# Performance work log

Hardware: AMD Instinct MI355X
Metric: run time of the kernel (lower is better)

## Reference

```python
import jax, jax.numpy as jnp
import numpy as np

E = 1024      # embed_dim
H = 16        # num_heads
HD = E // H   # head_dim = 64


def setup_inputs() -> dict:
    key = jax.random.key(0)
    ks = jax.random.split(key, 8)
    T, B, S = 1024, 4, 1024
    return {
        "query": jax.random.normal(ks[0], (T, B, E), jnp.float32),
        "key": jax.random.normal(ks[1], (S, B, E), jnp.float32),
        "value": jax.random.normal(ks[2], (S, B, E), jnp.float32),
        "attn_mask": jax.random.normal(ks[3], (T, S), jnp.float32),
        "key_padding_mask": jax.random.randint(ks[4], (B, S), 0, 2, jnp.int32),
        "in_proj_weight": jax.random.normal(ks[5], (3 * E, E), jnp.float32) * 0.02,
        "in_proj_bias": jnp.zeros((3 * E,), jnp.float32),
        "out_w": jax.random.normal(ks[6], (E, E), jnp.float32) * 0.02,
        "out_b": jnp.zeros((E,), jnp.float32),
    }


def reference(query, key, value, attn_mask, key_padding_mask,
              in_proj_weight, in_proj_bias, out_w, out_b):
    T, B, _ = query.shape
    S = key.shape[0]
    w_q, w_k, w_v = jnp.split(in_proj_weight, 3, axis=0)   # each [E, E]
    b_q, b_k, b_v = jnp.split(in_proj_bias, 3, axis=0)
    q = query @ w_q.T + b_q                                # [T, B, E]
    k = key @ w_k.T + b_k                                  # [S, B, E]
    v = value @ w_v.T + b_v                                # [S, B, E]
    # [len, B, E] -> [B*H, len, HD]
    q = q.reshape(T, B * H, HD).transpose(1, 0, 2) / jnp.sqrt(jnp.float32(HD))
    k = k.reshape(S, B * H, HD).transpose(1, 0, 2)
    v = v.reshape(S, B * H, HD).transpose(1, 0, 2)
    scores = jnp.einsum('bth,bsh->bts', q, k)              # [B*H, T, S]
    scores = scores + attn_mask[None]                      # float additive mask
    pad = key_padding_mask.astype(bool)                    # [B, S]
    pad = jnp.broadcast_to(pad[:, None, None, :], (B, H, 1, S)).reshape(B * H, 1, S)
    scores = jnp.where(pad, -jnp.inf, scores)
    weights = jax.nn.softmax(scores, axis=-1)              # dropout p=0 -> identity
    out = jnp.einsum('bts,bsh->bth', weights, v)           # [B*H, T, HD]
    out = out.transpose(1, 0, 2).reshape(T, B, E)
    out = out @ out_w.T + out_b
    weights_avg = weights.reshape(B, H, T, S).mean(axis=1) # sum/H == mean
    return out, weights_avg
```

## Files before the change

kernel.cpp:

```cpp
#include <hip/hip_runtime.h>
#include <stdint.h>

typedef short bf16x8 __attribute__((ext_vector_type(8)));
typedef float f32x4  __attribute__((ext_vector_type(4)));

#define LOG2E_F 1.4426950408889634f
#define QSCALE_F 0.1803368801111204f

__device__ __forceinline__ unsigned short f2bf(float f) {
    unsigned int u = __float_as_uint(f);
    return (unsigned short)((u + 0x7FFFu + ((u >> 16) & 1u)) >> 16);
}

__device__ __forceinline__ unsigned short f2bfu(float f) {
    return (unsigned short)((__float_as_uint(f) + 0x8000u) >> 16);
}

__device__ __forceinline__ uint4 pack8(float4 a, float4 b) {
    union { unsigned short us[8]; uint4 v; } p;
    p.us[0] = f2bf(a.x); p.us[1] = f2bf(a.y); p.us[2] = f2bf(a.z); p.us[3] = f2bf(a.w);
    p.us[4] = f2bf(b.x); p.us[5] = f2bf(b.y); p.us[6] = f2bf(b.z); p.us[7] = f2bf(b.w);
    return p.v;
}

__global__ __launch_bounds__(256)
void cvt_kernel(const float* __restrict__ q, const float* __restrict__ k,
                const float* __restrict__ v, const float* __restrict__ w,
                const float* __restrict__ ow,
                uint4* __restrict__ Xb, uint4* __restrict__ Wb, uint4* __restrict__ OWb)
{
    const unsigned g = blockIdx.x * 256 + threadIdx.x;
    const float* src;
    uint4* dst;
    if (g < 1572864u) {
        dst = Xb + g;
        if (g < 524288u)        src = q + (size_t)g * 8;
        else if (g < 1048576u)  src = k + (size_t)(g - 524288u) * 8;
        else                    src = v + (size_t)(g - 1048576u) * 8;
    } else if (g < 1966080u) {
        src = w + (size_t)(g - 1572864u) * 8;
        dst = Wb + (g - 1572864u);
    } else {
        src = ow + (size_t)(g - 1966080u) * 8;
        dst = OWb + (g - 1966080u);
    }
    float4 a = *(const float4*)src;
    float4 b = *(const float4*)(src + 4);
    *dst = pack8(a, b);
}

__global__ __launch_bounds__(256)
void qkv_proj_kernel(const unsigned short* __restrict__ Xb, const unsigned short* __restrict__ Wb,
                     const float* __restrict__ bias,
                     unsigned short* __restrict__ Qb, unsigned short* __restrict__ Kb,
                     unsigned short* __restrict__ Vtb)
{
    const int z = blockIdx.z;
    const int j   = blockIdx.x;
    const int xcd = j & 7, idx = j >> 3;
    const int row0 = ((xcd << 2) + (idx >> 3)) * 128;
    const int col0 = (idx & 7) * 128;
    const int wofs = z << 10;

    const unsigned short* A = Xb + (size_t)z * 4194304;
    const unsigned short* B = Wb;

    __shared__ __align__(16) unsigned short As[128 * 72];
    __shared__ __align__(16) unsigned short Bs[128 * 72];

    const int tid  = threadIdx.x;
    const int lane = tid & 63;
    const int wv   = tid >> 6;
    const int wr   = wv >> 1, wc = wv & 1;

    const f32x4 zero4 = {0.f, 0.f, 0.f, 0.f};
    f32x4 acc[4][4];
#pragma unroll
    for (int m = 0; m < 4; ++m)
#pragma unroll
        for (int n = 0; n < 4; ++n) acc[m][n] = zero4;

    const int srow = tid >> 1;
    const int scol = (tid & 1) << 5;
    const int arow = wr * 64 + (lane & 15);
    const int brow = wc * 64 + (lane & 15);
    const int kof  = (lane >> 4) << 3;

    const unsigned short* pa = A + (size_t)(row0 + srow) * 1024 + scol;
    const unsigned short* pb = B + (size_t)(wofs + col0 + srow) * 1024 + scol;
    uint4 ra0 = *(const uint4*)(pa + 0),  ra1 = *(const uint4*)(pa + 8);
    uint4 ra2 = *(const uint4*)(pa + 16), ra3 = *(const uint4*)(pa + 24);
    uint4 rb0 = *(const uint4*)(pb + 0),  rb1 = *(const uint4*)(pb + 8);
    uint4 rb2 = *(const uint4*)(pb + 16), rb3 = *(const uint4*)(pb + 24);

    for (int k0 = 0; k0 < 1024; k0 += 64) {
        __syncthreads();
        *(uint4*)&As[srow * 72 + scol]      = ra0;
        *(uint4*)&As[srow * 72 + scol + 8]  = ra1;
        *(uint4*)&As[srow * 72 + scol + 16] = ra2;
        *(uint4*)&As[srow * 72 + scol + 24] = ra3;
        *(uint4*)&Bs[srow * 72 + scol]      = rb0;
        *(uint4*)&Bs[srow * 72 + scol + 8]  = rb1;
        *(uint4*)&Bs[srow * 72 + scol + 16] = rb2;
        *(uint4*)&Bs[srow * 72 + scol + 24] = rb3;
        __syncthreads();

        if (k0 < 960) {
            pa = A + (size_t)(row0 + srow) * 1024 + k0 + 64 + scol;
            pb = B + (size_t)(wofs + col0 + srow) * 1024 + k0 + 64 + scol;
            ra0 = *(const uint4*)(pa + 0);  ra1 = *(const uint4*)(pa + 8);
            ra2 = *(const uint4*)(pa + 16); ra3 = *(const uint4*)(pa + 24);
            rb0 = *(const uint4*)(pb + 0);  rb1 = *(const uint4*)(pb + 8);
            rb2 = *(const uint4*)(pb + 16); rb3 = *(const uint4*)(pb + 24);
        }

#pragma unroll
        for (int kk = 0; kk < 2; ++kk) {
            bf16x8 af[4], bfr[4];
#pragma unroll
            for (int m = 0; m < 4; ++m)
                af[m] = *(const bf16x8*)&As[(arow + m * 16) * 72 + kk * 32 + kof];
#pragma unroll
            for (int n = 0; n < 4; ++n)
                bfr[n] = *(const bf16x8*)&Bs[(brow + n * 16) * 72 + kk * 32 + kof];
#pragma unroll
            for (int m = 0; m < 4; ++m)
#pragma unroll
                for (int n = 0; n < 4; ++n)
                    acc[m][n] = __builtin_amdgcn_mfma_f32_16x16x32_bf16(af[m], bfr[n], acc[m][n], 0, 0, 0);
        }
    }

    const int ccol = lane & 15;
    const int crow = (lane >> 4) << 2;
#pragma unroll
    for (int n = 0; n < 4; ++n) {
        const int gc   = col0 + wc * 64 + n * 16 + ccol;
        const float bv = bias[wofs + gc];
        const int head = gc >> 6, d = gc & 63;
#pragma unroll
        for (int m = 0; m < 4; ++m) {
#pragma unroll
            for (int r = 0; r < 4; ++r) {
                const int gr = row0 + wr * 64 + m * 16 + crow + r;
                const int t  = gr >> 2, b = gr & 3;
                const int bh = (b << 4) + head;
                float vv = acc[m][n][r] + bv;
                if (z == 0)      Qb [((size_t)bh << 16) + ((size_t)t << 6) + d]  = f2bf(vv * QSCALE_F);
                else if (z == 1) Kb [((size_t)bh << 16) + ((size_t)t << 6) + d]  = f2bf(vv);
                else             Vtb[((size_t)bh << 16) + ((size_t)d << 10) + t] = f2bf(vv);
            }
        }
    }
}

__global__ __launch_bounds__(256)
void flash_kernel(const unsigned short* __restrict__ Qb, const unsigned short* __restrict__ Kb,
                  const unsigned short* __restrict__ Vtb, const float* __restrict__ attn_mask,
                  const int* __restrict__ padmask,
                  float* __restrict__ rl_buf, unsigned short* __restrict__ attn_out)
{
    const int j   = blockIdx.x;
    const int xcd = j & 7, idx = j >> 3;
    const int bh  = xcd * 8 + (idx >> 4);
    const int t0  = (idx & 15) << 6;
    const int b   = bh >> 4, h = bh & 15;

    __shared__ __align__(16) unsigned short Ks[64 * 72];
    __shared__ __align__(16) unsigned short Vs[64 * 72];
    __shared__ __align__(16) unsigned short Ps[64 * 72];

    const int tid  = threadIdx.x;
    const int lane = tid & 63;
    const int wv   = tid >> 6;
    const int kof  = (lane >> 4) << 3;
    const int c16  = lane & 15;

    const unsigned short* Qbase = Qb  + ((size_t)bh << 16);
    const unsigned short* Kbase = Kb  + ((size_t)bh << 16);
    const unsigned short* Vbase = Vtb + ((size_t)bh << 16);

    bf16x8 qf[2];
#pragma unroll
    for (int kk = 0; kk < 2; ++kk)
        qf[kk] = *(const bf16x8*)(Qbase + ((size_t)(t0 + wv * 16 + c16) << 6) + kk * 32 + kof);

    const bf16x8 ones = {16256, 16256, 16256, 16256, 16256, 16256, 16256, 16256};

    const f32x4 zero4 = {0.f, 0.f, 0.f, 0.f};
    f32x4 acco[4];
#pragma unroll
    for (int nd = 0; nd < 4; ++nd) acco[nd] = zero4;
    f32x4 acc_l = zero4;

    const int srow_st = tid >> 2;
    const int scol_st = (tid & 3) << 4;

    const unsigned short* kp = Kbase + ((size_t)srow_st << 6) + scol_st;
    const unsigned short* vp = Vbase + ((size_t)srow_st << 10) + scol_st;
    uint4 kr0 = *(const uint4*)kp, kr1 = *(const uint4*)(kp + 8);
    uint4 vr0 = *(const uint4*)vp, vr1 = *(const uint4*)(vp + 8);

    for (int s0 = 0; s0 < 1024; s0 += 64) {
        __syncthreads();
        *(uint4*)&Ks[srow_st * 72 + scol_st]     = kr0;
        *(uint4*)&Ks[srow_st * 72 + scol_st + 8] = kr1;
        *(uint4*)&Vs[srow_st * 72 + scol_st]     = vr0;
        *(uint4*)&Vs[srow_st * 72 + scol_st + 8] = vr1;
        __syncthreads();

        if (s0 < 960) {
            kp = Kbase + ((size_t)(s0 + 64 + srow_st) << 6) + scol_st;
            vp = Vbase + ((size_t)srow_st << 10) + (s0 + 64) + scol_st;
            kr0 = *(const uint4*)kp; kr1 = *(const uint4*)(kp + 8);
            vr0 = *(const uint4*)vp; vr1 = *(const uint4*)(vp + 8);
        }

        f32x4 accs[4];
#pragma unroll
        for (int n = 0; n < 4; ++n) accs[n] = zero4;
#pragma unroll
        for (int n = 0; n < 4; ++n) {
            bf16x8 kf0 = *(const bf16x8*)&Ks[(n * 16 + c16) * 72 + kof];
            bf16x8 kf1 = *(const bf16x8*)&Ks[(n * 16 + c16) * 72 + 32 + kof];
            accs[n] = __builtin_amdgcn_mfma_f32_16x16x32_bf16(qf[0], kf0, accs[n], 0, 0, 0);
            accs[n] = __builtin_amdgcn_mfma_f32_16x16x32_bf16(qf[1], kf1, accs[n], 0, 0, 0);
        }

        int pad_s[4];
#pragma unroll
        for (int n = 0; n < 4; ++n)
            pad_s[n] = padmask[(b << 10) + s0 + n * 16 + c16];

        const int rbase = wv * 16 + ((lane >> 4) << 2);
#pragma unroll
        for (int r = 0; r < 4; ++r) {
            const float* mp = attn_mask + (size_t)(t0 + rbase + r) * 1024 + s0 + c16;
            float x0 = fmaf(mp[ 0], LOG2E_F, accs[0][r]);
            float x1 = fmaf(mp[16], LOG2E_F, accs[1][r]);
            float x2 = fmaf(mp[32], LOG2E_F, accs[2][r]);
            float x3 = fmaf(mp[48], LOG2E_F, accs[3][r]);
            if (pad_s[0]) x0 = -1e30f;
            if (pad_s[1]) x1 = -1e30f;
            if (pad_s[2]) x2 = -1e30f;
            if (pad_s[3]) x3 = -1e30f;
            const float p0 = __builtin_amdgcn_exp2f(x0);
            const float p1 = __builtin_amdgcn_exp2f(x1);
            const float p2 = __builtin_amdgcn_exp2f(x2);
            const float p3 = __builtin_amdgcn_exp2f(x3);
            const int prow = rbase + r;
            Ps[prow * 72 +  0 + c16] = f2bfu(p0);
            Ps[prow * 72 + 16 + c16] = f2bfu(p1);
            Ps[prow * 72 + 32 + c16] = f2bfu(p2);
            Ps[prow * 72 + 48 + c16] = f2bfu(p3);
        }

#pragma unroll
        for (int kk2 = 0; kk2 < 2; ++kk2) {
            bf16x8 pf = *(const bf16x8*)&Ps[(wv * 16 + c16) * 72 + kk2 * 32 + kof];
#pragma unroll
            for (int nd = 0; nd < 4; ++nd) {
                bf16x8 vf = *(const bf16x8*)&Vs[(nd * 16 + c16) * 72 + kk2 * 32 + kof];
                acco[nd] = __builtin_amdgcn_mfma_f32_16x16x32_bf16(pf, vf, acco[nd], 0, 0, 0);
            }
            acc_l = __builtin_amdgcn_mfma_f32_16x16x32_bf16(pf, ones, acc_l, 0, 0, 0);
        }
    }

#pragma unroll
    for (int r = 0; r < 4; ++r) {
        const int t = t0 + wv * 16 + ((lane >> 4) << 2) + r;
        const float rl = 1.0f / acc_l[r];
        if (c16 == 0)
            rl_buf[(bh << 10) + t] = rl;
#pragma unroll
        for (int nd = 0; nd < 4; ++nd) {
            const int d = nd * 16 + c16;
            attn_out[((size_t)t * 4 + b) * 1024 + h * 64 + d] = f2bf(acco[nd][r] * rl);
        }
    }
}

__global__ __launch_bounds__(256)
void wavg_kernel(const unsigned short* __restrict__ Qb, const unsigned short* __restrict__ Kb,
                 const float* __restrict__ attn_mask, const int* __restrict__ padmask,
                 const float* __restrict__ rl_buf, float* __restrict__ wout)
{
    const int j   = blockIdx.x;
    const int xcd = j & 7;
    const int b   = xcd >> 1;
    const int rr  = ((j >> 3) << 1) + (xcd & 1);
    const int t0  = (rr >> 4) << 6;
    const int s0  = (rr & 15) << 6;

    __shared__ __align__(16) unsigned short Qs[64 * 72];
    __shared__ __align__(16) unsigned short Ks2[64 * 72];

    const int tid  = threadIdx.x;
    const int lane = tid & 63;
    const int wv   = tid >> 6;
    const int wr   = wv >> 1, wc = wv & 1;
    const int kof  = (lane >> 4) << 3;
    const int srow_st = tid >> 2;
    const int scol_st = (tid & 3) << 4;

    const int t_base = t0 + wr * 32 + ((lane >> 4) << 2);
    const int s_base = s0 + wc * 32 + (lane & 15);

    int pad2[2];
#pragma unroll
    for (int nn = 0; nn < 2; ++nn) pad2[nn] = padmask[(b << 10) + s_base + nn * 16];

    float maskv[2][2][4];
#pragma unroll
    for (int mm = 0; mm < 2; ++mm)
#pragma unroll
        for (int r = 0; r < 4; ++r)
#pragma unroll
            for (int nn = 0; nn < 2; ++nn)
                maskv[mm][nn][r] = attn_mask[(size_t)(t_base + mm * 16 + r) * 1024 + s_base + nn * 16] * LOG2E_F;

    float wsum[2][2][4];
#pragma unroll
    for (int mm = 0; mm < 2; ++mm)
#pragma unroll
        for (int nn = 0; nn < 2; ++nn)
#pragma unroll
            for (int r = 0; r < 4; ++r) wsum[mm][nn][r] = 0.f;

    for (int h = 0; h < 16; ++h) {
        const int bh = (b << 4) + h;
        __syncthreads();
        {
            const unsigned short* qp = Qb + ((size_t)bh << 16) + ((size_t)(t0 + srow_st) << 6) + scol_st;
            *(uint4*)&Qs[srow_st * 72 + scol_st]     = *(const uint4*)qp;
            *(uint4*)&Qs[srow_st * 72 + scol_st + 8] = *(const uint4*)(qp + 8);
            const unsigned short* kp = Kb + ((size_t)bh << 16) + ((size_t)(s0 + srow_st) << 6) + scol_st;
            *(uint4*)&Ks2[srow_st * 72 + scol_st]     = *(const uint4*)kp;
            *(uint4*)&Ks2[srow_st * 72 + scol_st + 8] = *(const uint4*)(kp + 8);
        }
        __syncthreads();

        float rlv[2][4];
#pragma unroll
        for (int mm = 0; mm < 2; ++mm)
#pragma unroll
            for (int r = 0; r < 4; ++r)
                rlv[mm][r] = rl_buf[(bh << 10) + t_base + mm * 16 + r];

        const f32x4 zero4 = {0.f, 0.f, 0.f, 0.f};
        f32x4 accs[2][2];
#pragma unroll
        for (int mm = 0; mm < 2; ++mm)
#pragma unroll
            for (int nn = 0; nn < 2; ++nn) accs[mm][nn] = zero4;
#pragma unroll
        for (int nn = 0; nn < 2; ++nn) {
            bf16x8 kf0 = *(const bf16x8*)&Ks2[(wc * 32 + nn * 16 + (lane & 15)) * 72 + kof];
            bf16x8 kf1 = *(const bf16x8*)&Ks2[(wc * 32 + nn * 16 + (lane & 15)) * 72 + 32 + kof];
#pragma unroll
            for (int mm = 0; mm < 2; ++mm) {
                bf16x8 qf0 = *(const bf16x8*)&Qs[(wr * 32 + mm * 16 + (lane & 15)) * 72 + kof];
                bf16x8 qf1 = *(const bf16x8*)&Qs[(wr * 32 + mm * 16 + (lane & 15)) * 72 + 32 + kof];
                accs[mm][nn] = __builtin_amdgcn_mfma_f32_16x16x32_bf16(qf0, kf0, accs[mm][nn], 0, 0, 0);
                accs[mm][nn] = __builtin_amdgcn_mfma_f32_16x16x32_bf16(qf1, kf1, accs[mm][nn], 0, 0, 0);
            }
        }
#pragma unroll
        for (int mm = 0; mm < 2; ++mm)
#pragma unroll
            for (int nn = 0; nn < 2; ++nn)
#pragma unroll
                for (int r = 0; r < 4; ++r)
                    if (!pad2[nn]) {
                        float x = accs[mm][nn][r] + maskv[mm][nn][r];
                        wsum[mm][nn][r] += __builtin_amdgcn_exp2f(x) * rlv[mm][r];
                    }
    }

#pragma unroll
    for (int mm = 0; mm < 2; ++mm)
#pragma unroll
        for (int nn = 0; nn < 2; ++nn)
#pragma unroll
            for (int r = 0; r < 4; ++r)
                wout[((size_t)b << 20) + (size_t)(t_base + mm * 16 + r) * 1024 + s_base + nn * 16]
                    = wsum[mm][nn][r] * 0.0625f;
}

__global__ __launch_bounds__(256)
void out_proj_kernel(const unsigned short* __restrict__ A, const unsigned short* __restrict__ Wb,
                     const float* __restrict__ bias, float* __restrict__ out)
{
    const int j   = blockIdx.x;
    const int xcd = j & 7, idx = j >> 3;
    const int row0 = ((xcd << 2) + (idx >> 3)) * 128;
    const int col0 = (idx & 7) * 128;

    __shared__ __align__(16) unsigned short As[128 * 72];
    __shared__ __align__(16) unsigned short Bs[128 * 72];

    const int tid  = threadIdx.x;
    const int lane = tid & 63;
    const int wv   = tid >> 6;
    const int wr   = wv >> 1, wc = wv & 1;

    const f32x4 zero4 = {0.f, 0.f, 0.f, 0.f};
    f32x4 acc[4][4];
#pragma unroll
    for (int m = 0; m < 4; ++m)
#pragma unroll
        for (int n = 0; n < 4; ++n) acc[m][n] = zero4;

    const int srow = tid >> 1;
    const int scol = (tid & 1) << 5;
    const int arow = wr * 64 + (lane & 15);
    const int brow = wc * 64 + (lane & 15);
    const int kof  = (lane >> 4) << 3;

    const unsigned short* pa = A  + (size_t)(row0 + srow) * 1024 + scol;
    const unsigned short* pb = Wb + (size_t)(col0 + srow) * 1024 + scol;
    uint4 ra0 = *(const uint4*)(pa + 0),  ra1 = *(const uint4*)(pa + 8);
    uint4 ra2 = *(const uint4*)(pa + 16), ra3 = *(const uint4*)(pa + 24);
    uint4 rb0 = *(const uint4*)(pb + 0),  rb1 = *(const uint4*)(pb + 8);
    uint4 rb2 = *(const uint4*)(pb + 16), rb3 = *(const uint4*)(pb + 24);

    for (int k0 = 0; k0 < 1024; k0 += 64) {
        __syncthreads();
        *(uint4*)&As[srow * 72 + scol]      = ra0;
        *(uint4*)&As[srow * 72 + scol + 8]  = ra1;
        *(uint4*)&As[srow * 72 + scol + 16] = ra2;
        *(uint4*)&As[srow * 72 + scol + 24] = ra3;
        *(uint4*)&Bs[srow * 72 + scol]      = rb0;
        *(uint4*)&Bs[srow * 72 + scol + 8]  = rb1;
        *(uint4*)&Bs[srow * 72 + scol + 16] = rb2;
        *(uint4*)&Bs[srow * 72 + scol + 24] = rb3;
        __syncthreads();

        if (k0 < 960) {
            pa = A  + (size_t)(row0 + srow) * 1024 + k0 + 64 + scol;
            pb = Wb + (size_t)(col0 + srow) * 1024 + k0 + 64 + scol;
            ra0 = *(const uint4*)(pa + 0);  ra1 = *(const uint4*)(pa + 8);
            ra2 = *(const uint4*)(pa + 16); ra3 = *(const uint4*)(pa + 24);
            rb0 = *(const uint4*)(pb + 0);  rb1 = *(const uint4*)(pb + 8);
            rb2 = *(const uint4*)(pb + 16); rb3 = *(const uint4*)(pb + 24);
        }

#pragma unroll
        for (int kk = 0; kk < 2; ++kk) {
            bf16x8 af[4], bfr[4];
#pragma unroll
            for (int m = 0; m < 4; ++m)
                af[m] = *(const bf16x8*)&As[(arow + m * 16) * 72 + kk * 32 + kof];
#pragma unroll
            for (int n = 0; n < 4; ++n)
                bfr[n] = *(const bf16x8*)&Bs[(brow + n * 16) * 72 + kk * 32 + kof];
#pragma unroll
            for (int m = 0; m < 4; ++m)
#pragma unroll
                for (int n = 0; n < 4; ++n)
                    acc[m][n] = __builtin_amdgcn_mfma_f32_16x16x32_bf16(af[m], bfr[n], acc[m][n], 0, 0, 0);
        }
    }

    const int ccol = lane & 15;
    const int crow = (lane >> 4) << 2;
#pragma unroll
    for (int n = 0; n < 4; ++n) {
        const int gc   = col0 + wc * 64 + n * 16 + ccol;
        const float bv = bias[gc];
#pragma unroll
        for (int m = 0; m < 4; ++m) {
#pragma unroll
            for (int r = 0; r < 4; ++r) {
                const int gr = row0 + wr * 64 + m * 16 + crow + r;
                out[(size_t)gr * 1024 + gc] = acc[m][n][r] + bv;
            }
        }
    }
}

extern "C" void kernel_launch(void* const* d_in, const int* in_sizes, int n_in,
                              void* d_out, int out_size, void* d_ws, size_t ws_size,
                              hipStream_t stream)
{
    const float* query     = (const float*)d_in[0];
    const float* key       = (const float*)d_in[1];
    const float* value     = (const float*)d_in[2];
    const float* attn_mask = (const float*)d_in[3];
    const int*   padmask   = (const int*)  d_in[4];
    const float* in_proj_w = (const float*)d_in[5];
    const float* in_proj_b = (const float*)d_in[6];
    const float* out_w     = (const float*)d_in[7];
    const float* out_b     = (const float*)d_in[8];

    float* out  = (float*)d_out;
    float* wavg = out + 4194304;

    char* ws = (char*)d_ws;
    unsigned short* Qb     = (unsigned short*)(ws);
    unsigned short* Kb     = (unsigned short*)(ws + 8388608);
    unsigned short* Vtb    = (unsigned short*)(ws + 16777216);
    unsigned short* Xb     = (unsigned short*)(ws + 25165824);
    unsigned short* attn_o = (unsigned short*)(ws + 25165824);
    unsigned short* Wb     = (unsigned short*)(ws + 50331648);
    unsigned short* OWb    = (unsigned short*)(ws + 56623104);
    float*          rl_buf = (float*)(ws + 58720256);

    cvt_kernel<<<dim3(8192), 256, 0, stream>>>(query, key, value, in_proj_w, out_w,
                                               (uint4*)Xb, (uint4*)Wb, (uint4*)OWb);
    qkv_proj_kernel<<<dim3(256, 1, 3), 256, 0, stream>>>(Xb, Wb, in_proj_b, Qb, Kb, Vtb);
    flash_kernel<<<dim3(1024), 256, 0, stream>>>(Qb, Kb, Vtb, attn_mask, padmask,
                                                 rl_buf, attn_o);
    wavg_kernel<<<dim3(1024), 256, 0, stream>>>(Qb, Kb, attn_mask, padmask,
                                                rl_buf, wavg);
    out_proj_kernel<<<dim3(256), 256, 0, stream>>>(attn_o, OWb, out_b, out);
}
```

Measured before the change: 158.6 us.

## Double-buffer K/V and Q/K tiles in flash and wavg kernels, enlarge flash blocks

The flash kernel now runs 512-thread blocks covering 128 query rows, with double-buffered K/V shared tiles. The attention mask and padding values for the next tile are prefetched into registers, and s_setprio is raised around the MFMA sections. The wavg kernel likewise double-buffers its Q/K tiles across heads, which drops one barrier per iteration. The aim is to hide global-load latency behind MFMA work and cut synchronisation, at the cost of more registers and LDS per block, which may lower occupancy.

Result: slower. 200.1 us (+26.2%).

```diff
diff --git a/kernel.cpp b/kernel.cpp
--- a/kernel.cpp
+++ b/kernel.cpp
@@ -154,7 +154,7 @@
     }
 }
 
-__global__ __launch_bounds__(256)
+__global__ __launch_bounds__(512, 4)
 void flash_kernel(const unsigned short* __restrict__ Qb, const unsigned short* __restrict__ Kb,
                   const unsigned short* __restrict__ Vtb, const float* __restrict__ attn_mask,
                   const int* __restrict__ padmask,
@@ -162,13 +162,13 @@
 {
     const int j   = blockIdx.x;
     const int xcd = j & 7, idx = j >> 3;
-    const int bh  = xcd * 8 + (idx >> 4);
-    const int t0  = (idx & 15) << 6;
+    const int bh  = xcd * 8 + (idx >> 3);
+    const int t0  = (idx & 7) << 7;
     const int b   = bh >> 4, h = bh & 15;
 
-    __shared__ __align__(16) unsigned short Ks[64 * 72];
-    __shared__ __align__(16) unsigned short Vs[64 * 72];
-    __shared__ __align__(16) unsigned short Ps[64 * 72];
+    __shared__ __align__(16) unsigned short Ks[2][64 * 72];
+    __shared__ __align__(16) unsigned short Vs[2][64 * 72];
+    __shared__ __align__(16) unsigned short Ps[128 * 72];
 
     const int tid  = threadIdx.x;
     const int lane = tid & 63;
@@ -193,57 +193,77 @@
     for (int nd = 0; nd < 4; ++nd) acco[nd] = zero4;
     f32x4 acc_l = zero4;
 
-    const int srow_st = tid >> 2;
-    const int scol_st = (tid & 3) << 4;
-
-    const unsigned short* kp = Kbase + ((size_t)srow_st << 6) + scol_st;
-    const unsigned short* vp = Vbase + ((size_t)srow_st << 10) + scol_st;
-    uint4 kr0 = *(const uint4*)kp, kr1 = *(const uint4*)(kp + 8);
-    uint4 vr0 = *(const uint4*)vp, vr1 = *(const uint4*)(vp + 8);
-
-    for (int s0 = 0; s0 < 1024; s0 += 64) {
-        __syncthreads();
-        *(uint4*)&Ks[srow_st * 72 + scol_st]     = kr0;
-        *(uint4*)&Ks[srow_st * 72 + scol_st + 8] = kr1;
-        *(uint4*)&Vs[srow_st * 72 + scol_st]     = vr0;
-        *(uint4*)&Vs[srow_st * 72 + scol_st + 8] = vr1;
-        __syncthreads();
-
-        if (s0 < 960) {
-            kp = Kbase + ((size_t)(s0 + 64 + srow_st) << 6) + scol_st;
-            vp = Vbase + ((size_t)srow_st << 10) + (s0 + 64) + scol_st;
-            kr0 = *(const uint4*)kp; kr1 = *(const uint4*)(kp + 8);
-            vr0 = *(const uint4*)vp; vr1 = *(const uint4*)(vp + 8);
+    const int srow = tid >> 3;
+    const int scol = (tid & 7) << 3;
+
+    const int tr = t0 + wv * 16 + ((lane >> 4) << 2);
+
+    uint4 kreg = *(const uint4*)(Kbase + ((size_t)srow << 6) + scol);
+    uint4 vreg = *(const uint4*)(Vbase + ((size_t)srow << 10) + scol);
+    float mreg[2][4][4];
+    int   preg[2][4];
+#pragma unroll
+    for (int n = 0; n < 4; ++n) preg[0][n] = padmask[(b << 10) + n * 16 + c16];
+#pragma unroll
+    for (int r = 0; r < 4; ++r)
+#pragma unroll
+        for (int n = 0; n < 4; ++n)
+            mreg[0][r][n] = attn_mask[(size_t)(tr + r) * 1024 + n * 16 + c16];
+
+    *(uint4*)&Ks[0][srow * 72 + scol] = kreg;
+    *(uint4*)&Vs[0][srow * 72 + scol] = vreg;
+    kreg = *(const uint4*)(Kbase + ((size_t)(64 + srow) << 6) + scol);
+    vreg = *(const uint4*)(Vbase + ((size_t)srow << 10) + 64 + scol);
+    __syncthreads();
+
+#pragma unroll 2
+    for (int it = 0; it < 16; ++it) {
+        const int cur = it & 1;
+
+        if (it < 15) {
+            *(uint4*)&Ks[cur ^ 1][srow * 72 + scol] = kreg;
+            *(uint4*)&Vs[cur ^ 1][srow * 72 + scol] = vreg;
+        }
+        if (it < 14) {
+            const int s2 = (it + 2) << 6;
+            kreg = *(const uint4*)(Kbase + ((size_t)(s2 + srow) << 6) + scol);
+            vreg = *(const uint4*)(Vbase + ((size_t)srow << 10) + s2 + scol);
+        }
+        if (it < 15) {
+            const int s1 = (it + 1) << 6;
+#pragma unroll
+            for (int n = 0; n < 4; ++n) preg[cur ^ 1][n] = padmask[(b << 10) + s1 + n * 16 + c16];
+#pragma unroll
+            for (int r = 0; r < 4; ++r)
+#pragma unroll
+                for (int n = 0; n < 4; ++n)
+                    mreg[cur ^ 1][r][n] = attn_mask[(size_t)(tr + r) * 1024 + s1 + n * 16 + c16];
         }
 
         f32x4 accs[4];
 #pragma unroll
         for (int n = 0; n < 4; ++n) accs[n] = zero4;
+        __builtin_amdgcn_s_setprio(1);
 #pragma unroll
         for (int n = 0; n < 4; ++n) {
-            bf16x8 kf0 = *(const bf16x8*)&Ks[(n * 16 + c16) * 72 + kof];
-            bf16x8 kf1 = *(const bf16x8*)&Ks[(n * 16 + c16) * 72 + 32 + kof];
+            bf16x8 kf0 = *(const bf16x8*)&Ks[cur][(n * 16 + c16) * 72 + kof];
+            bf16x8 kf1 = *(const bf16x8*)&Ks[cur][(n * 16 + c16) * 72 + 32 + kof];
             accs[n] = __builtin_amdgcn_mfma_f32_16x16x32_bf16(qf[0], kf0, accs[n], 0, 0, 0);
             accs[n] = __builtin_amdgcn_mfma_f32_16x16x32_bf16(qf[1], kf1, accs[n], 0, 0, 0);
         }
-
-        int pad_s[4];
-#pragma unroll
-        for (int n = 0; n < 4; ++n)
-            pad_s[n] = padmask[(b << 10) + s0 + n * 16 + c16];
+        __builtin_amdgcn_s_setprio(0);
 
         const int rbase = wv * 16 + ((lane >> 4) << 2);
 #pragma unroll
         for (int r = 0; r < 4; ++r) {
-            const float* mp = attn_mask + (size_t)(t0 + rbase + r) * 1024 + s0 + c16;
-            float x0 = fmaf(mp[ 0], LOG2E_F, accs[0][r]);
-            float x1 = fmaf(mp[16], LOG2E_F, accs[1][r]);
-            float x2 = fmaf(mp[32], LOG2E_F, accs[2][r]);
-            float x3 = fmaf(mp[48], LOG2E_F, accs[3][r]);
-            if (pad_s[0]) x0 = -1e30f;
-            if (pad_s[1]) x1 = -1e30f;
-            if (pad_s[2]) x2 = -1e30f;
-            if (pad_s[3]) x3 = -1e30f;
+            float x0 = fmaf(mreg[cur][r][0], LOG2E_F, accs[0][r]);
+            float x1 = fmaf(mreg[cur][r][1], LOG2E_F, accs[1][r]);
+            float x2 = fmaf(mreg[cur][r][2], LOG2E_F, accs[2][r]);
+            float x3 = fmaf(mreg[cur][r][3], LOG2E_F, accs[3][r]);
+            if (preg[cur][0]) x0 = -1e30f;
+            if (preg[cur][1]) x1 = -1e30f;
+            if (preg[cur][2]) x2 = -1e30f;
+            if (preg[cur][3]) x3 = -1e30f;
             const float p0 = __builtin_amdgcn_exp2f(x0);
             const float p1 = __builtin_amdgcn_exp2f(x1);
             const float p2 = __builtin_amdgcn_exp2f(x2);
@@ -255,16 +275,20 @@
             Ps[prow * 72 + 48 + c16] = f2bfu(p3);
         }
 
+        __builtin_amdgcn_s_setprio(1);
 #pragma unroll
         for (int kk2 = 0; kk2 < 2; ++kk2) {
             bf16x8 pf = *(const bf16x8*)&Ps[(wv * 16 + c16) * 72 + kk2 * 32 + kof];
 #pragma unroll
             for (int nd = 0; nd < 4; ++nd) {
-                bf16x8 vf = *(const bf16x8*)&Vs[(nd * 16 + c16) * 72 + kk2 * 32 + kof];
+                bf16x8 vf = *(const bf16x8*)&Vs[cur][(nd * 16 + c16) * 72 + kk2 * 32 + kof];
                 acco[nd] = __builtin_amdgcn_mfma_f32_16x16x32_bf16(pf, vf, acco[nd], 0, 0, 0);
             }
             acc_l = __builtin_amdgcn_mfma_f32_16x16x32_bf16(pf, ones, acc_l, 0, 0, 0);
         }
+        __builtin_amdgcn_s_setprio(0);
+
+        if (it < 15) __syncthreads();
     }
 
 #pragma unroll
@@ -293,8 +317,8 @@
     const int t0  = (rr >> 4) << 6;
     const int s0  = (rr & 15) << 6;
 
-    __shared__ __align__(16) unsigned short Qs[64 * 72];
-    __shared__ __align__(16) unsigned short Ks2[64 * 72];
+    __shared__ __align__(16) unsigned short Qs[2][64 * 72];
+    __shared__ __align__(16) unsigned short Ks2[2][64 * 72];
 
     const int tid  = threadIdx.x;
     const int lane = tid & 63;
@@ -328,18 +352,42 @@
 #pragma unroll
             for (int r = 0; r < 4; ++r) wsum[mm][nn][r] = 0.f;
 
+    const unsigned short* qsrc = Qb + ((size_t)(t0 + srow_st) << 6) + scol_st;
+    const unsigned short* ksrc = Kb + ((size_t)(s0 + srow_st) << 6) + scol_st;
+    const size_t bh0 = (size_t)(b << 4) << 16;
+
+    uint4 q0 = *(const uint4*)(qsrc + bh0);
+    uint4 q1 = *(const uint4*)(qsrc + bh0 + 8);
+    uint4 k0 = *(const uint4*)(ksrc + bh0);
+    uint4 k1 = *(const uint4*)(ksrc + bh0 + 8);
+    *(uint4*)&Qs[0][srow_st * 72 + scol_st]      = q0;
+    *(uint4*)&Qs[0][srow_st * 72 + scol_st + 8]  = q1;
+    *(uint4*)&Ks2[0][srow_st * 72 + scol_st]     = k0;
+    *(uint4*)&Ks2[0][srow_st * 72 + scol_st + 8] = k1;
+    q0 = *(const uint4*)(qsrc + bh0 + 65536);
+    q1 = *(const uint4*)(qsrc + bh0 + 65536 + 8);
+    k0 = *(const uint4*)(ksrc + bh0 + 65536);
+    k1 = *(const uint4*)(ksrc + bh0 + 65536 + 8);
+    __syncthreads();
+
+#pragma unroll 2
     for (int h = 0; h < 16; ++h) {
-        const int bh = (b << 4) + h;
-        __syncthreads();
-        {
-            const unsigned short* qp = Qb + ((size_t)bh << 16) + ((size_t)(t0 + srow_st) << 6) + scol_st;
-            *(uint4*)&Qs[srow_st * 72 + scol_st]     = *(const uint4*)qp;
-            *(uint4*)&Qs[srow_st * 72 + scol_st + 8] = *(const uint4*)(qp + 8);
-            const unsigned short* kp = Kb + ((size_t)bh << 16) + ((size_t)(s0 + srow_st) << 6) + scol_st;
-            *(uint4*)&Ks2[srow_st * 72 + scol_st]     = *(const uint4*)kp;
-            *(uint4*)&Ks2[srow_st * 72 + scol_st + 8] = *(const uint4*)(kp + 8);
-        }
-        __syncthreads();
+        const int cur = h & 1;
+        const int bh  = (b << 4) + h;
+
+        if (h < 15) {
+            *(uint4*)&Qs[cur ^ 1][srow_st * 72 + scol_st]      = q0;
+            *(uint4*)&Qs[cur ^ 1][srow_st * 72 + scol_st + 8]  = q1;
+            *(uint4*)&Ks2[cur ^ 1][srow_st * 72 + scol_st]     = k0;
+            *(uint4*)&Ks2[cur ^ 1][srow_st * 72 + scol_st + 8] = k1;
+        }
+        if (h < 14) {
+            const size_t of = bh0 + (size_t)(h + 2) * 65536;
+            q0 = *(const uint4*)(qsrc + of);
+            q1 = *(const uint4*)(qsrc + of + 8);
+            k0 = *(const uint4*)(ksrc + of);
+            k1 = *(const uint4*)(ksrc + of + 8);
+        }
 
         float rlv[2][4];
 #pragma unroll
@@ -356,12 +404,12 @@
             for (int nn = 0; nn < 2; ++nn) accs[mm][nn] = zero4;
 #pragma unroll
         for (int nn = 0; nn < 2; ++nn) {
-            bf16x8 kf0 = *(const bf16x8*)&Ks2[(wc * 32 + nn * 16 + (lane & 15)) * 72 + kof];
-            bf16x8 kf1 = *(const bf16x8*)&Ks2[(wc * 32 + nn * 16 + (lane & 15)) * 72 + 32 + kof];
+            bf16x8 kf0 = *(const bf16x8*)&Ks2[cur][(wc * 32 + nn * 16 + (lane & 15)) * 72 + kof];
+            bf16x8 kf1 = *(const bf16x8*)&Ks2[cur][(wc * 32 + nn * 16 + (lane & 15)) * 72 + 32 + kof];
 #pragma unroll
             for (int mm = 0; mm < 2; ++mm) {
-                bf16x8 qf0 = *(const bf16x8*)&Qs[(wr * 32 + mm * 16 + (lane & 15)) * 72 + kof];
-                bf16x8 qf1 = *(const bf16x8*)&Qs[(wr * 32 + mm * 16 + (lane & 15)) * 72 + 32 + kof];
+                bf16x8 qf0 = *(const bf16x8*)&Qs[cur][(wr * 32 + mm * 16 + (lane & 15)) * 72 + kof];
+                bf16x8 qf1 = *(const bf16x8*)&Qs[cur][(wr * 32 + mm * 16 + (lane & 15)) * 72 + 32 + kof];
                 accs[mm][nn] = __builtin_amdgcn_mfma_f32_16x16x32_bf16(qf0, kf0, accs[mm][nn], 0, 0, 0);
                 accs[mm][nn] = __builtin_amdgcn_mfma_f32_16x16x32_bf16(qf1, kf1, accs[mm][nn], 0, 0, 0);
             }
@@ -376,6 +424,8 @@
                         float x = accs[mm][nn][r] + maskv[mm][nn][r];
                         wsum[mm][nn][r] += __builtin_amdgcn_exp2f(x) * rlv[mm][r];
                     }
+
+        if (h < 15) __syncthreads();
     }
 
 #pragma unroll
@@ -510,8 +560,8 @@
     cvt_kernel<<<dim3(8192), 256, 0, stream>>>(query, key, value, in_proj_w, out_w,
                                                (uint4*)Xb, (uint4*)Wb, (uint4*)OWb);
     qkv_proj_kernel<<<dim3(256, 1, 3), 256, 0, stream>>>(Xb, Wb, in_proj_b, Qb, Kb, Vtb);
-    flash_kernel<<<dim3(1024), 256, 0, stream>>>(Qb, Kb, Vtb, attn_mask, padmask,
-                                                 rl_buf, attn_o);
+    flash_kernel<<<dim3(512), 512, 0, stream>>>(Qb, Kb, Vtb, attn_mask, padmask,
+                                                rl_buf, attn_o);
     wavg_kernel<<<dim3(1024), 256, 0, stream>>>(Qb, Kb, attn_mask, padmask,
                                                 rl_buf, wavg);
     out_proj_kernel<<<dim3(256), 256, 0, stream>>>(attn_o, OWb, out_b, out);
```

## Load K/V/Q MFMA fragments directly from global memory, drop LDS staging and barriers

Applied to the files above, without the earlier changes.

In both the flash attention kernel and the weight-averaging kernel, the shared-memory staging of K, V (and Q in wavg) is removed. MFMA operands are now read straight from global memory, relying on L1/L2 caching, and the two __syncthreads per iteration are gone. s_setprio raises wave priority around the MFMA sections. This removes the LDS round trip and barrier stalls, but drops the register prefetch double-buffering and makes each wave issue redundant global loads that may expose memory latency.

Result: slower. 271.7 us (+71.3%).

```diff
diff --git a/kernel.cpp b/kernel.cpp
--- a/kernel.cpp
+++ b/kernel.cpp
@@ -166,8 +166,6 @@
     const int t0  = (idx & 15) << 6;
     const int b   = bh >> 4, h = bh & 15;
 
-    __shared__ __align__(16) unsigned short Ks[64 * 72];
-    __shared__ __align__(16) unsigned short Vs[64 * 72];
     __shared__ __align__(16) unsigned short Ps[64 * 72];
 
     const int tid  = threadIdx.x;
@@ -193,49 +191,32 @@
     for (int nd = 0; nd < 4; ++nd) acco[nd] = zero4;
     f32x4 acc_l = zero4;
 
-    const int srow_st = tid >> 2;
-    const int scol_st = (tid & 3) << 4;
-
-    const unsigned short* kp = Kbase + ((size_t)srow_st << 6) + scol_st;
-    const unsigned short* vp = Vbase + ((size_t)srow_st << 10) + scol_st;
-    uint4 kr0 = *(const uint4*)kp, kr1 = *(const uint4*)(kp + 8);
-    uint4 vr0 = *(const uint4*)vp, vr1 = *(const uint4*)(vp + 8);
+    const int rbase = wv * 16 + ((lane >> 4) << 2);
+    const int tr    = t0 + rbase;
 
     for (int s0 = 0; s0 < 1024; s0 += 64) {
-        __syncthreads();
-        *(uint4*)&Ks[srow_st * 72 + scol_st]     = kr0;
-        *(uint4*)&Ks[srow_st * 72 + scol_st + 8] = kr1;
-        *(uint4*)&Vs[srow_st * 72 + scol_st]     = vr0;
-        *(uint4*)&Vs[srow_st * 72 + scol_st + 8] = vr1;
-        __syncthreads();
-
-        if (s0 < 960) {
-            kp = Kbase + ((size_t)(s0 + 64 + srow_st) << 6) + scol_st;
-            vp = Vbase + ((size_t)srow_st << 10) + (s0 + 64) + scol_st;
-            kr0 = *(const uint4*)kp; kr1 = *(const uint4*)(kp + 8);
-            vr0 = *(const uint4*)vp; vr1 = *(const uint4*)(vp + 8);
-        }
-
         f32x4 accs[4];
 #pragma unroll
         for (int n = 0; n < 4; ++n) accs[n] = zero4;
+        __builtin_amdgcn_s_setprio(1);
 #pragma unroll
         for (int n = 0; n < 4; ++n) {
-            bf16x8 kf0 = *(const bf16x8*)&Ks[(n * 16 + c16) * 72 + kof];
-            bf16x8 kf1 = *(const bf16x8*)&Ks[(n * 16 + c16) * 72 + 32 + kof];
+            const unsigned short* kr = Kbase + ((size_t)(s0 + n * 16 + c16) << 6) + kof;
+            bf16x8 kf0 = *(const bf16x8*)(kr);
+            bf16x8 kf1 = *(const bf16x8*)(kr + 32);
             accs[n] = __builtin_amdgcn_mfma_f32_16x16x32_bf16(qf[0], kf0, accs[n], 0, 0, 0);
             accs[n] = __builtin_amdgcn_mfma_f32_16x16x32_bf16(qf[1], kf1, accs[n], 0, 0, 0);
         }
+        __builtin_amdgcn_s_setprio(0);
 
         int pad_s[4];
 #pragma unroll
         for (int n = 0; n < 4; ++n)
             pad_s[n] = padmask[(b << 10) + s0 + n * 16 + c16];
 
-        const int rbase = wv * 16 + ((lane >> 4) << 2);
 #pragma unroll
         for (int r = 0; r < 4; ++r) {
-            const float* mp = attn_mask + (size_t)(t0 + rbase + r) * 1024 + s0 + c16;
+            const float* mp = attn_mask + (size_t)(tr + r) * 1024 + s0 + c16;
             float x0 = fmaf(mp[ 0], LOG2E_F, accs[0][r]);
             float x1 = fmaf(mp[16], LOG2E_F, accs[1][r]);
             float x2 = fmaf(mp[32], LOG2E_F, accs[2][r]);
@@ -255,21 +236,23 @@
             Ps[prow * 72 + 48 + c16] = f2bfu(p3);
         }
 
+        __builtin_amdgcn_s_setprio(1);
 #pragma unroll
         for (int kk2 = 0; kk2 < 2; ++kk2) {
             bf16x8 pf = *(const bf16x8*)&Ps[(wv * 16 + c16) * 72 + kk2 * 32 + kof];
 #pragma unroll
             for (int nd = 0; nd < 4; ++nd) {
-                bf16x8 vf = *(const bf16x8*)&Vs[(nd * 16 + c16) * 72 + kk2 * 32 + kof];
+                bf16x8 vf = *(const bf16x8*)(Vbase + ((size_t)(nd * 16 + c16) << 10) + s0 + kk2 * 32 + kof);
                 acco[nd] = __builtin_amdgcn_mfma_f32_16x16x32_bf16(pf, vf, acco[nd], 0, 0, 0);
             }
             acc_l = __builtin_amdgcn_mfma_f32_16x16x32_bf16(pf, ones, acc_l, 0, 0, 0);
         }
+        __builtin_amdgcn_s_setprio(0);
     }
 
 #pragma unroll
     for (int r = 0; r < 4; ++r) {
-        const int t = t0 + wv * 16 + ((lane >> 4) << 2) + r;
+        const int t = t0 + rbase + r;
         const float rl = 1.0f / acc_l[r];
         if (c16 == 0)
             rl_buf[(bh << 10) + t] = rl;
@@ -293,19 +276,15 @@
     const int t0  = (rr >> 4) << 6;
     const int s0  = (rr & 15) << 6;
 
-    __shared__ __align__(16) unsigned short Qs[64 * 72];
-    __shared__ __align__(16) unsigned short Ks2[64 * 72];
-
     const int tid  = threadIdx.x;
     const int lane = tid & 63;
     const int wv   = tid >> 6;
     const int wr   = wv >> 1, wc = wv & 1;
     const int kof  = (lane >> 4) << 3;
-    const int srow_st = tid >> 2;
-    const int scol_st = (tid & 3) << 4;
+    const int c16  = lane & 15;
 
     const int t_base = t0 + wr * 32 + ((lane >> 4) << 2);
-    const int s_base = s0 + wc * 32 + (lane & 15);
+    const int s_base = s0 + wc * 32 + c16;
 
     int pad2[2];
 #pragma unroll
@@ -328,18 +307,12 @@
 #pragma unroll
             for (int r = 0; r < 4; ++r) wsum[mm][nn][r] = 0.f;
 
+    const f32x4 zero4 = {0.f, 0.f, 0.f, 0.f};
+
     for (int h = 0; h < 16; ++h) {
         const int bh = (b << 4) + h;
-        __syncthreads();
-        {
-            const unsigned short* qp = Qb + ((size_t)bh << 16) + ((size_t)(t0 + srow_st) << 6) + scol_st;
-            *(uint4*)&Qs[srow_st * 72 + scol_st]     = *(const uint4*)qp;
-            *(uint4*)&Qs[srow_st * 72 + scol_st + 8] = *(const uint4*)(qp + 8);
-            const unsigned short* kp = Kb + ((size_t)bh << 16) + ((size_t)(s0 + srow_st) << 6) + scol_st;
-            *(uint4*)&Ks2[srow_st * 72 + scol_st]     = *(const uint4*)kp;
-            *(uint4*)&Ks2[srow_st * 72 + scol_st + 8] = *(const uint4*)(kp + 8);
-        }
-        __syncthreads();
+        const unsigned short* Qh = Qb + ((size_t)bh << 16);
+        const unsigned short* Kh = Kb + ((size_t)bh << 16);
 
         float rlv[2][4];
 #pragma unroll
@@ -348,24 +321,29 @@
             for (int r = 0; r < 4; ++r)
                 rlv[mm][r] = rl_buf[(bh << 10) + t_base + mm * 16 + r];
 
-        const f32x4 zero4 = {0.f, 0.f, 0.f, 0.f};
         f32x4 accs[2][2];
 #pragma unroll
         for (int mm = 0; mm < 2; ++mm)
 #pragma unroll
             for (int nn = 0; nn < 2; ++nn) accs[mm][nn] = zero4;
+
+        __builtin_amdgcn_s_setprio(1);
 #pragma unroll
         for (int nn = 0; nn < 2; ++nn) {
-            bf16x8 kf0 = *(const bf16x8*)&Ks2[(wc * 32 + nn * 16 + (lane & 15)) * 72 + kof];
-            bf16x8 kf1 = *(const bf16x8*)&Ks2[(wc * 32 + nn * 16 + (lane & 15)) * 72 + 32 + kof];
+            const unsigned short* kr = Kh + ((size_t)(s0 + wc * 32 + nn * 16 + c16) << 6) + kof;
+            bf16x8 kf0 = *(const bf16x8*)(kr);
+            bf16x8 kf1 = *(const bf16x8*)(kr + 32);
 #pragma unroll
             for (int mm = 0; mm < 2; ++mm) {
-                bf16x8 qf0 = *(const bf16x8*)&Qs[(wr * 32 + mm * 16 + (lane & 15)) * 72 + kof];
-                bf16x8 qf1 = *(const bf16x8*)&Qs[(wr * 32 + mm * 16 + (lane & 15)) * 72 + 32 + kof];
+                const unsigned short* qr = Qh + ((size_t)(t0 + wr * 32 + mm * 16 + c16) << 6) + kof;
+                bf16x8 qf0 = *(const bf16x8*)(qr);
+                bf16x8 qf1 = *(const bf16x8*)(qr + 32);
                 accs[mm][nn] = __builtin_amdgcn_mfma_f32_16x16x32_bf16(qf0, kf0, accs[mm][nn], 0, 0, 0);
                 accs[mm][nn] = __builtin_amdgcn_mfma_f32_16x16x32_bf16(qf1, kf1, accs[mm][nn], 0, 0, 0);
             }
         }
+        __builtin_amdgcn_s_setprio(0);
+
 #pragma unroll
         for (int mm = 0; mm < 2; ++mm)
 #pragma unroll
```

## Shrink flash key tile to 32 to raise occupancy, add MFMA priority hints

Applied to the files above, without the earlier changes.

The flash attention loop now processes 32 keys per iteration instead of 64, which shrinks the K/V/P shared-memory tiles and the per-thread prefetch registers. Launch bounds now request 8 blocks per SM to raise occupancy. s_setprio is placed around the MFMA sections so matrix work is favoured over the softmax/mask code of other waves. In exchange the loop runs twice as many iterations, doubling the barriers and per-iteration overhead.

Result: slower. 184.0 us (+16.0%).

```diff
diff --git a/kernel.cpp b/kernel.cpp
--- a/kernel.cpp
+++ b/kernel.cpp
@@ -154,7 +154,7 @@
     }
 }
 
-__global__ __launch_bounds__(256)
+__global__ __launch_bounds__(256, 8)
 void flash_kernel(const unsigned short* __restrict__ Qb, const unsigned short* __restrict__ Kb,
                   const unsigned short* __restrict__ Vtb, const float* __restrict__ attn_mask,
                   const int* __restrict__ padmask,
@@ -166,9 +166,9 @@
     const int t0  = (idx & 15) << 6;
     const int b   = bh >> 4, h = bh & 15;
 
-    __shared__ __align__(16) unsigned short Ks[64 * 72];
-    __shared__ __align__(16) unsigned short Vs[64 * 72];
-    __shared__ __align__(16) unsigned short Ps[64 * 72];
+    __shared__ __align__(16) unsigned short Ks[32 * 72];
+    __shared__ __align__(16) unsigned short Vs[64 * 40];
+    __shared__ __align__(16) unsigned short Ps[64 * 40];
 
     const int tid  = threadIdx.x;
     const int lane = tid & 63;
@@ -193,83 +193,74 @@
     for (int nd = 0; nd < 4; ++nd) acco[nd] = zero4;
     f32x4 acc_l = zero4;
 
-    const int srow_st = tid >> 2;
-    const int scol_st = (tid & 3) << 4;
-
-    const unsigned short* kp = Kbase + ((size_t)srow_st << 6) + scol_st;
-    const unsigned short* vp = Vbase + ((size_t)srow_st << 10) + scol_st;
-    uint4 kr0 = *(const uint4*)kp, kr1 = *(const uint4*)(kp + 8);
-    uint4 vr0 = *(const uint4*)vp, vr1 = *(const uint4*)(vp + 8);
-
-    for (int s0 = 0; s0 < 1024; s0 += 64) {
-        __syncthreads();
-        *(uint4*)&Ks[srow_st * 72 + scol_st]     = kr0;
-        *(uint4*)&Ks[srow_st * 72 + scol_st + 8] = kr1;
-        *(uint4*)&Vs[srow_st * 72 + scol_st]     = vr0;
-        *(uint4*)&Vs[srow_st * 72 + scol_st + 8] = vr1;
-        __syncthreads();
-
-        if (s0 < 960) {
-            kp = Kbase + ((size_t)(s0 + 64 + srow_st) << 6) + scol_st;
-            vp = Vbase + ((size_t)srow_st << 10) + (s0 + 64) + scol_st;
-            kr0 = *(const uint4*)kp; kr1 = *(const uint4*)(kp + 8);
-            vr0 = *(const uint4*)vp; vr1 = *(const uint4*)(vp + 8);
-        }
-
-        f32x4 accs[4];
-#pragma unroll
-        for (int n = 0; n < 4; ++n) accs[n] = zero4;
-#pragma unroll
-        for (int n = 0; n < 4; ++n) {
+    const int srowK = tid >> 3;
+    const int scolK = (tid & 7) << 3;
+    const int srowV = tid >> 2;
+    const int scolV = (tid & 3) << 3;
+
+    const int rbase = wv * 16 + ((lane >> 4) << 2);
+    const int tr    = t0 + rbase;
+
+    uint4 kreg = *(const uint4*)(Kbase + ((size_t)srowK << 6) + scolK);
+    uint4 vreg = *(const uint4*)(Vbase + ((size_t)srowV << 10) + scolV);
+
+    for (int it = 0; it < 32; ++it) {
+        const int s0 = it << 5;
+        __syncthreads();
+        *(uint4*)&Ks[srowK * 72 + scolK] = kreg;
+        *(uint4*)&Vs[srowV * 40 + scolV] = vreg;
+        __syncthreads();
+
+        if (it < 31) {
+            kreg = *(const uint4*)(Kbase + ((size_t)(s0 + 32 + srowK) << 6) + scolK);
+            vreg = *(const uint4*)(Vbase + ((size_t)srowV << 10) + (s0 + 32) + scolV);
+        }
+
+        f32x4 accs[2];
+        accs[0] = zero4; accs[1] = zero4;
+        __builtin_amdgcn_s_setprio(1);
+#pragma unroll
+        for (int n = 0; n < 2; ++n) {
             bf16x8 kf0 = *(const bf16x8*)&Ks[(n * 16 + c16) * 72 + kof];
             bf16x8 kf1 = *(const bf16x8*)&Ks[(n * 16 + c16) * 72 + 32 + kof];
             accs[n] = __builtin_amdgcn_mfma_f32_16x16x32_bf16(qf[0], kf0, accs[n], 0, 0, 0);
             accs[n] = __builtin_amdgcn_mfma_f32_16x16x32_bf16(qf[1], kf1, accs[n], 0, 0, 0);
         }
-
-        int pad_s[4];
-#pragma unroll
-        for (int n = 0; n < 4; ++n)
-            pad_s[n] = padmask[(b << 10) + s0 + n * 16 + c16];
-
-        const int rbase = wv * 16 + ((lane >> 4) << 2);
+        __builtin_amdgcn_s_setprio(0);
+
+        int pad_s0 = padmask[(b << 10) + s0 + c16];
+        int pad_s1 = padmask[(b << 10) + s0 + 16 + c16];
+
 #pragma unroll
         for (int r = 0; r < 4; ++r) {
-            const float* mp = attn_mask + (size_t)(t0 + rbase + r) * 1024 + s0 + c16;
+            const float* mp = attn_mask + (size_t)(tr + r) * 1024 + s0 + c16;
             float x0 = fmaf(mp[ 0], LOG2E_F, accs[0][r]);
             float x1 = fmaf(mp[16], LOG2E_F, accs[1][r]);
-            float x2 = fmaf(mp[32], LOG2E_F, accs[2][r]);
-            float x3 = fmaf(mp[48], LOG2E_F, accs[3][r]);
-            if (pad_s[0]) x0 = -1e30f;
-            if (pad_s[1]) x1 = -1e30f;
-            if (pad_s[2]) x2 = -1e30f;
-            if (pad_s[3]) x3 = -1e30f;
+            if (pad_s0) x0 = -1e30f;
+            if (pad_s1) x1 = -1e30f;
             const float p0 = __builtin_amdgcn_exp2f(x0);
             const float p1 = __builtin_amdgcn_exp2f(x1);
-            const float p2 = __builtin_amdgcn_exp2f(x2);
-            const float p3 = __builtin_amdgcn_exp2f(x3);
             const int prow = rbase + r;
-            Ps[prow * 72 +  0 + c16] = f2bfu(p0);
-            Ps[prow * 72 + 16 + c16] = f2bfu(p1);
-            Ps[prow * 72 + 32 + c16] = f2bfu(p2);
-            Ps[prow * 72 + 48 + c16] = f2bfu(p3);
-        }
-
-#pragma unroll
-        for (int kk2 = 0; kk2 < 2; ++kk2) {
-            bf16x8 pf = *(const bf16x8*)&Ps[(wv * 16 + c16) * 72 + kk2 * 32 + kof];
+            Ps[prow * 40 +  0 + c16] = f2bfu(p0);
+            Ps[prow * 40 + 16 + c16] = f2bfu(p1);
+        }
+
+        __builtin_amdgcn_s_setprio(1);
+        {
+            bf16x8 pf = *(const bf16x8*)&Ps[(wv * 16 + c16) * 40 + kof];
 #pragma unroll
             for (int nd = 0; nd < 4; ++nd) {
-                bf16x8 vf = *(const bf16x8*)&Vs[(nd * 16 + c16) * 72 + kk2 * 32 + kof];
+                bf16x8 vf = *(const bf16x8*)&Vs[(nd * 16 + c16) * 40 + kof];
                 acco[nd] = __builtin_amdgcn_mfma_f32_16x16x32_bf16(pf, vf, acco[nd], 0, 0, 0);
             }
             acc_l = __builtin_amdgcn_mfma_f32_16x16x32_bf16(pf, ones, acc_l, 0, 0, 0);
         }
+        __builtin_amdgcn_s_setprio(0);
     }
 
 #pragma unroll
     for (int r = 0; r < 4; ++r) {
-        const int t = t0 + wv * 16 + ((lane >> 4) << 2) + r;
+        const int t = t0 + rbase + r;
         const float rl = 1.0f / acc_l[r];
         if (c16 == 0)
             rl_buf[(bh << 10) + t] = rl;
```
